# Performance work log

Measured on AMD Instinct MI355X. Metric: run time of the kernel, lower is better.

## Reference

```python
import jax, jax.numpy as jnp
import numpy as np

S, B, E, H, M = 1024, 4, 1024, 16, 128  # seq, batch, embed, heads, model_dims (key width)
V = E // H                              # value_dims = 64
_WSCALE = 1.0 / np.sqrt(E)              # keep softmax logits O(1)


def _cplx(re, im):
    return jax.lax.complex(re, im)


def setup_inputs() -> dict:
    key = jax.random.key(0)
    ks = jax.random.split(key, 10)
    n = lambda k, shp: jax.random.normal(k, shp, dtype=jnp.float32)
    w = lambda k, shp: n(k, shp) * np.float32(_WSCALE / np.sqrt(2.0))
    return {
        "logits_re": n(ks[0], (S, B, E)),
        "logits_im": n(ks[1], (S, B, E)),
        "wq_re": w(ks[2], (H, M, E)), "wq_im": w(ks[3], (H, M, E)),
        "wk_re": w(ks[4], (H, M, E)), "wk_im": w(ks[5], (H, M, E)),
        "wv_re": w(ks[6], (H, V, E)), "wv_im": w(ks[7], (H, V, E)),
        "wo_re": w(ks[8], (E, E)),    "wo_im": w(ks[9], (E, E)),
    }


def reference(logits_re, logits_im, wq_re, wq_im, wk_re, wk_im,
              wv_re, wv_im, wo_re, wo_im):
    x = _cplx(logits_re, logits_im)          # (s, b, e) complex64
    wq = _cplx(wq_re, wq_im)                 # (h, m, e)
    wk = _cplx(wk_re, wk_im)
    wv = _cplx(wv_re, wv_im)                 # (h, v, e)
    wo = _cplx(wo_re, wo_im)                 # (e, e)

    q = jnp.einsum('hme,sbe->bhsm', wq, x)   # (b, h, s, m)
    k = jnp.einsum('hme,sbe->bhsm', wk, x)
    v = jnp.einsum('hve,sbe->bhsv', wv, x)   # (b, h, s, v)

    scores = jnp.einsum('bhsm,bhtm->bhst', q, k)         # complex, no conjugation (matches torch matmul)
    amp = jnp.abs(scores)                                # -> float32
    causal = jnp.triu(jnp.ones((S, S), dtype=bool), 1)   # True above diagonal -> masked
    amp = jnp.where(causal, -jnp.inf, amp) / jnp.sqrt(jnp.float32(M))
    attn = jax.nn.softmax(amp, axis=-1).astype(scores.dtype)  # cast back to complex64

    upd = jnp.einsum('bhst,bhtv->bhsv', attn, v)         # (b, h, s, v)
    upd = upd.transpose(2, 0, 1, 3).reshape(S, B, E)     # 's2 b (h v)'
    out = jnp.einsum('sbe,ef->sbf', upd, wo) + x         # residual
    # complex output returned as stacked (real, imag) float32 for harness compatibility
    return jnp.stack([out.real, out.imag])
```

## Files before the change

kernel.cpp:

```cpp
#include <hip/hip_runtime.h>
#include <math.h>

#define S_DIM 1024
#define B_DIM 4
#define E_DIM 1024
#define H_DIM 16
#define M_DIM 128
#define V_DIM 64

typedef __attribute__((ext_vector_type(8))) short short8;
typedef __attribute__((ext_vector_type(4))) float f32x4;
typedef __attribute__((ext_vector_type(4))) int int4v;

__device__ __forceinline__ unsigned short f2bf(float f) {
    union { float f; unsigned u; } v; v.f = f;
    unsigned r = v.u + 0x7FFFu + ((v.u >> 16) & 1u);
    return (unsigned short)(r >> 16);
}

__device__ __forceinline__ void async16(const unsigned short* g, unsigned short* l) {
    __builtin_amdgcn_global_load_lds(
        (const __attribute__((address_space(1))) void*)g,
        (__attribute__((address_space(3))) void*)l,
        16, 0, 0);
}

__global__ __launch_bounds__(256) void convert_all(
    const float* __restrict__ xre,  const float* __restrict__ xim,
    const float* __restrict__ wqre, const float* __restrict__ wqim,
    const float* __restrict__ wkre, const float* __restrict__ wkim,
    const float* __restrict__ wvre, const float* __restrict__ wvim,
    unsigned short* __restrict__ xbre, unsigned short* __restrict__ xbim,
    unsigned short* __restrict__ wbre, unsigned short* __restrict__ wbim)
{
    const int i = blockIdx.x * 256 + threadIdx.x;
    const float *re, *im;
    unsigned short *dr, *di;
    int j;
    if (i < 1048576)      { re = xre;  im = xim;  dr = xbre;               di = xbim;               j = i; }
    else if (i < 1572864) { re = wqre; im = wqim; dr = wbre;               di = wbim;               j = i - 1048576; }
    else if (i < 2097152) { re = wkre; im = wkim; dr = wbre + 2048 * 1024; di = wbim + 2048 * 1024; j = i - 1572864; }
    else                  { re = wvre; im = wvim; dr = wbre + 4096 * 1024; di = wbim + 4096 * 1024; j = i - 2097152; }
    float4 r = ((const float4*)re)[j];
    float4 m = ((const float4*)im)[j];
    ushort4 ro, mo;
    ro.x = f2bf(r.x); ro.y = f2bf(r.y); ro.z = f2bf(r.z); ro.w = f2bf(r.w);
    mo.x = f2bf(m.x); mo.y = f2bf(m.y); mo.z = f2bf(m.z); mo.w = f2bf(m.w);
    ((ushort4*)dr)[j] = ro;
    ((ushort4*)di)[j] = mo;
}

__global__ __launch_bounds__(256) void transpose_wo(
    const float* __restrict__ wore, const float* __restrict__ woim,
    unsigned short* __restrict__ wtre, unsigned short* __restrict__ wtim)
{
    __shared__ float tr[32][33], ti[32][33];
    const int bx = blockIdx.x * 32;
    const int by = blockIdx.y * 32;
    const int tx = threadIdx.x & 31, ty = threadIdx.x >> 5;
    for (int i = ty; i < 32; i += 8) {
        tr[i][tx] = wore[(bx + i) * E_DIM + by + tx];
        ti[i][tx] = woim[(bx + i) * E_DIM + by + tx];
    }
    __syncthreads();
    for (int i = ty; i < 32; i += 8) {
        wtre[(by + i) * E_DIM + bx + tx] = f2bf(tr[tx][i]);
        wtim[(by + i) * E_DIM + bx + tx] = f2bf(ti[tx][i]);
    }
}

__global__ __launch_bounds__(256) void vtrans(
    const unsigned short* __restrict__ vrp, const unsigned short* __restrict__ vip,
    unsigned short* __restrict__ vrt, unsigned short* __restrict__ vit)
{
    __shared__ unsigned short tl[2][64][66];
    const int tid = threadIdx.x;
    const int t0 = blockIdx.x * 64;
    const int bh = blockIdx.y;
    #pragma unroll
    for (int pl = 0; pl < 2; ++pl) {
        const unsigned short* src = pl ? vip : vrp;
        #pragma unroll
        for (int p = 0; p < 2; ++p) {
            const int row = p * 32 + (tid >> 3);
            const int col = (tid & 7) * 8;
            short8 d = *(const short8*)&src[((size_t)bh * S_DIM + t0 + row) * V_DIM + col];
            #pragma unroll
            for (int j = 0; j < 8; ++j) tl[pl][row][col + j] = (unsigned short)d[j];
        }
    }
    __syncthreads();
    #pragma unroll
    for (int pl = 0; pl < 2; ++pl) {
        unsigned short* dst = pl ? vit : vrt;
        #pragma unroll
        for (int p = 0; p < 2; ++p) {
            const int v = p * 32 + (tid >> 3);
            const int tc = (tid & 7) * 8;
            short8 d;
            #pragma unroll
            for (int j = 0; j < 8; ++j) d[j] = (short)tl[pl][tc + j][v];
            *(short8*)&dst[((size_t)bh * V_DIM + v) * S_DIM + t0 + tc] = d;
        }
    }
}

template<int MODE>
__global__ __launch_bounds__(256, MODE ? 3 : 2) void cgemm(
    const unsigned short* __restrict__ Are, const unsigned short* __restrict__ Aim,
    const unsigned short* __restrict__ Bre, const unsigned short* __restrict__ Bim,
    unsigned short* __restrict__ qrp, unsigned short* __restrict__ qip,
    unsigned short* __restrict__ krp, unsigned short* __restrict__ kip,
    unsigned short* __restrict__ vrp, unsigned short* __restrict__ vip,
    const float* __restrict__ xre, const float* __restrict__ xim,
    float* __restrict__ out)
{
    constexpr int BM  = MODE ? 64 : 128;
    constexpr int IM  = MODE ? 2 : 4;
    constexpr int ASZ = BM * 32;
    constexpr int BUF = 2 * ASZ + 8192;
    __shared__ __align__(16) unsigned short lds[2 * BUF];
    const int tid  = threadIdx.x;
    const int wave = tid >> 6;
    const int lane = tid & 63;
    const int r0 = blockIdx.x * BM;
    const int j0 = blockIdx.y * 128;
    const int wm = (wave >> 1) * (MODE ? 32 : 64);
    const int wn = (wave & 1) * 64;

    f32x4 accre[IM][4], accim[IM][4];
    #pragma unroll
    for (int i = 0; i < IM; ++i)
        #pragma unroll
        for (int j = 0; j < 4; ++j) {
            accre[i][j] = (f32x4){0.f, 0.f, 0.f, 0.f};
            accim[i][j] = (f32x4){0.f, 0.f, 0.f, 0.f};
        }

    const int sr   = tid >> 2;
    const int sc   = (tid & 3) * 8;
    const int scol = ((tid & 3) ^ ((tid >> 3) & 3)) * 8;

    const int fr = lane & 15;
    const int xc = ((lane >> 4) ^ ((lane >> 1) & 3)) * 8;

    #define STAGE(sl, bb) { \
        const int kg = (sl) * 32; \
        unsigned short* b_ = &lds[(bb) * BUF]; \
        const size_t ga0 = (size_t)(r0 + sr) * E_DIM + kg + scol; \
        const size_t gb0 = (size_t)(j0 + sr) * E_DIM + kg + scol; \
        const size_t gb1 = (size_t)(j0 + 64 + sr) * E_DIM + kg + scol; \
        async16(Are + ga0, b_ + sr * 32 + sc); \
        async16(Aim + ga0, b_ + ASZ + sr * 32 + sc); \
        if (MODE == 0) { \
            const size_t ga1 = (size_t)(r0 + 64 + sr) * E_DIM + kg + scol; \
            async16(Are + ga1, b_ + (64 + sr) * 32 + sc); \
            async16(Aim + ga1, b_ + ASZ + (64 + sr) * 32 + sc); \
        } \
        async16(Bre + gb0, b_ + 2 * ASZ + sr * 32 + sc); \
        async16(Bre + gb1, b_ + 2 * ASZ + (64 + sr) * 32 + sc); \
        async16(Bim + gb0, b_ + 2 * ASZ + 4096 + sr * 32 + sc); \
        async16(Bim + gb1, b_ + 2 * ASZ + 4096 + (64 + sr) * 32 + sc); }

    STAGE(0, 0)
    asm volatile("s_waitcnt vmcnt(0)" ::: "memory");
    __builtin_amdgcn_s_barrier();

    #pragma unroll 1
    for (int s = 0; s < 32; ++s) {
        if (s < 31) STAGE(s + 1, (s + 1) & 1)

        const unsigned short* buf = &lds[(s & 1) * BUF];
        short8 ar[IM], ai[IM];
        #pragma unroll
        for (int im = 0; im < IM; ++im) {
            const int ro = (wm + im * 16 + fr) * 32 + xc;
            ar[im] = *(const short8*)&buf[ro];
            ai[im] = *(const short8*)&buf[ASZ + ro];
        }
        #pragma unroll
        for (int jn = 0; jn < 4; ++jn) {
            const int ro = (wn + jn * 16 + fr) * 32 + xc;
            const short8 br = *(const short8*)&buf[2 * ASZ + ro];
            const short8 bi = *(const short8*)&buf[2 * ASZ + 4096 + ro];
            int4v t = *(int4v*)&bi;
            t = t ^ (int)0x80008000;
            const short8 bin = *(short8*)&t;
            #pragma unroll
            for (int im = 0; im < IM; ++im) {
                accre[im][jn] = __builtin_amdgcn_mfma_f32_16x16x32_bf16(ar[im], br,  accre[im][jn], 0, 0, 0);
                accre[im][jn] = __builtin_amdgcn_mfma_f32_16x16x32_bf16(ai[im], bin, accre[im][jn], 0, 0, 0);
                accim[im][jn] = __builtin_amdgcn_mfma_f32_16x16x32_bf16(ar[im], bi,  accim[im][jn], 0, 0, 0);
                accim[im][jn] = __builtin_amdgcn_mfma_f32_16x16x32_bf16(ai[im], br,  accim[im][jn], 0, 0, 0);
            }
        }

        if (s < 31) {
            asm volatile("s_waitcnt vmcnt(0)" ::: "memory");
            __builtin_amdgcn_s_barrier();
        }
    }
    #undef STAGE

    const float qscale = 0.088388347648318447f;
    #pragma unroll
    for (int im = 0; im < IM; ++im) {
        #pragma unroll
        for (int reg = 0; reg < 4; ++reg) {
            const int r = r0 + wm + im * 16 + (lane >> 4) * 4 + reg;
            #pragma unroll
            for (int jn = 0; jn < 4; ++jn) {
                const int j = j0 + wn + jn * 16 + fr;
                const float vr = accre[im][jn][reg];
                const float vi = accim[im][jn][reg];
                if (MODE == 0) {
                    const int s = r >> 2, b = r & 3;
                    if (j < 2048) {
                        const int h = j >> 7, m = j & 127;
                        const size_t off = ((size_t)(b * H_DIM + h) * S_DIM + s) * M_DIM + m;
                        qrp[off] = f2bf(vr * qscale); qip[off] = f2bf(vi * qscale);
                    } else if (j < 4096) {
                        const int jl = j - 2048, h = jl >> 7, m = jl & 127;
                        const size_t off = ((size_t)(b * H_DIM + h) * S_DIM + s) * M_DIM + m;
                        krp[off] = f2bf(vr); kip[off] = f2bf(vi);
                    } else {
                        const int jl = j - 4096, h = jl >> 6, vv = jl & 63;
                        const size_t off = ((size_t)(b * H_DIM + h) * S_DIM + s) * V_DIM + vv;
                        vrp[off] = f2bf(vr); vip[off] = f2bf(vi);
                    }
                } else {
                    const int idx = r * E_DIM + j;
                    out[idx] = vr + xre[idx];
                    out[S_DIM * B_DIM * E_DIM + idx] = vi + xim[idx];
                }
            }
        }
    }
}

__global__ __launch_bounds__(512, 4) void attn_mfma(
    const unsigned short* __restrict__ qr, const unsigned short* __restrict__ qi,
    const unsigned short* __restrict__ kr, const unsigned short* __restrict__ ki,
    const unsigned short* __restrict__ vrt, const unsigned short* __restrict__ vit,
    unsigned short* __restrict__ updre, unsigned short* __restrict__ updim)
{
    __shared__ __align__(16) unsigned short Ks[2][64][136];
    __shared__ __align__(16) unsigned short Vs[2][64][72];
    __shared__ __align__(16) unsigned short Ps[8][16][88];

    const int tid  = threadIdx.x;
    const int wave = tid >> 6;
    const int lane = tid & 63;

    const int n  = blockIdx.x + 8 * blockIdx.y;
    const int bh = (n & 7) + 8 * (n >> 6);
    const int qt = 7 - ((n >> 3) & 7);

    const int q0 = qt * 128;
    const size_t base_qk = (size_t)bh * S_DIM * M_DIM;
    const size_t base_v  = (size_t)bh * V_DIM * S_DIM;

    const int fr = lane & 15;
    const int fg = lane >> 4;
    const int fk = fg * 8;

    const int krow = tid >> 4, kcol = (tid & 15) * 8;
    const int vrow = tid >> 3, vcol = (tid & 7) * 8;

    short8 Bqr[4], Bqi[4];
    {
        const size_t qo = base_qk + (size_t)(q0 + wave * 16 + fr) * M_DIM + fk;
        #pragma unroll
        for (int ks = 0; ks < 4; ++ks) {
            Bqr[ks] = *(const short8*)&qr[qo + ks * 32];
            Bqi[ks] = *(const short8*)&qi[qo + ks * 32];
        }
    }

    f32x4 Ore[4], Oim[4];
    #pragma unroll
    for (int vt = 0; vt < 4; ++vt) {
        Ore[vt] = (f32x4){0.f, 0.f, 0.f, 0.f};
        Oim[vt] = (f32x4){0.f, 0.f, 0.f, 0.f};
    }
    float mrun = -INFINITY, lrun = 0.f;
    const int qglob = q0 + wave * 16 + fr;
    const int qcap  = q0 + (wave >> 2) * 64;

    short8 pk[2][2], pv[2];
    #pragma unroll
    for (int pl = 0; pl < 2; ++pl) {
        const unsigned short* src = pl ? ki : kr;
        #pragma unroll
        for (int p = 0; p < 2; ++p)
            pk[pl][p] = *(const short8*)&src[base_qk + (size_t)(p * 32 + krow) * M_DIM + kcol];
    }
    #pragma unroll
    for (int pl = 0; pl < 2; ++pl) {
        const unsigned short* src = pl ? vit : vrt;
        pv[pl] = *(const short8*)&src[base_v + (size_t)vrow * S_DIM + vcol];
    }

    for (int t0 = 0; t0 <= q0 + 64; t0 += 64) {
        __syncthreads();
        #pragma unroll
        for (int pl = 0; pl < 2; ++pl) {
            #pragma unroll
            for (int p = 0; p < 2; ++p)
                *(short8*)&Ks[pl][p * 32 + krow][kcol] = pk[pl][p];
            *(short8*)&Vs[pl][vrow][vcol] = pv[pl];
        }
        __syncthreads();

        if (t0 <= q0) {
            const int tn = t0 + 64;
            #pragma unroll
            for (int pl = 0; pl < 2; ++pl) {
                const unsigned short* src = pl ? ki : kr;
                #pragma unroll
                for (int p = 0; p < 2; ++p)
                    pk[pl][p] = *(const short8*)&src[base_qk + (size_t)(tn + p * 32 + krow) * M_DIM + kcol];
            }
            #pragma unroll
            for (int pl = 0; pl < 2; ++pl) {
                const unsigned short* src = pl ? vit : vrt;
                pv[pl] = *(const short8*)&src[base_v + (size_t)vrow * S_DIM + tn + vcol];
            }
        }

        if (t0 > qcap) continue;

        f32x4 Sre[4], Sim[4];
        __builtin_amdgcn_s_setprio(1);
        #pragma unroll
        for (int tt = 0; tt < 4; ++tt) {
            Sre[tt] = (f32x4){0.f, 0.f, 0.f, 0.f};
            Sim[tt] = (f32x4){0.f, 0.f, 0.f, 0.f};
            const int trow = tt * 16 + fr;
            #pragma unroll
            for (int ks = 0; ks < 4; ++ks) {
                const short8 Akr = *(const short8*)&Ks[0][trow][ks * 32 + fk];
                const short8 Aki = *(const short8*)&Ks[1][trow][ks * 32 + fk];
                int4v t = *(int4v*)&Aki;
                t = t ^ (int)0x80008000;
                const short8 Akin = *(short8*)&t;
                Sre[tt] = __builtin_amdgcn_mfma_f32_16x16x32_bf16(Akr,  Bqr[ks], Sre[tt], 0, 0, 0);
                Sre[tt] = __builtin_amdgcn_mfma_f32_16x16x32_bf16(Akin, Bqi[ks], Sre[tt], 0, 0, 0);
                Sim[tt] = __builtin_amdgcn_mfma_f32_16x16x32_bf16(Akr,  Bqi[ks], Sim[tt], 0, 0, 0);
                Sim[tt] = __builtin_amdgcn_mfma_f32_16x16x32_bf16(Aki,  Bqr[ks], Sim[tt], 0, 0, 0);
            }
        }
        __builtin_amdgcn_s_setprio(0);

        float rowmax = -INFINITY;
        #pragma unroll
        for (int tt = 0; tt < 4; ++tt) {
            #pragma unroll
            for (int r = 0; r < 4; ++r) {
                const int tg = t0 + tt * 16 + fg * 4 + r;
                const float re = Sre[tt][r], im = Sim[tt][r];
                const float a = sqrtf(re * re + im * im);
                const float av = (tg > qglob) ? -INFINITY : a;
                Sre[tt][r] = av;
                rowmax = fmaxf(rowmax, av);
            }
        }
        rowmax = fmaxf(rowmax, __shfl_xor(rowmax, 16));
        rowmax = fmaxf(rowmax, __shfl_xor(rowmax, 32));

        if (!__all(rowmax - mrun <= 8.0f)) {
            const float nm = fmaxf(mrun, rowmax);
            const float alpha = __expf(mrun - nm);
            mrun = nm;
            lrun *= alpha;
            #pragma unroll
            for (int vt = 0; vt < 4; ++vt)
                #pragma unroll
                for (int r = 0; r < 4; ++r) { Ore[vt][r] *= alpha; Oim[vt][r] *= alpha; }
        }

        float psum = 0.f;
        #pragma unroll
        for (int tt = 0; tt < 4; ++tt) {
            const float p0 = __expf(Sre[tt][0] - mrun);
            const float p1 = __expf(Sre[tt][1] - mrun);
            const float p2 = __expf(Sre[tt][2] - mrun);
            const float p3 = __expf(Sre[tt][3] - mrun);
            psum += p0 + p1 + p2 + p3;
            ushort4 pw;
            pw.x = f2bf(p0); pw.y = f2bf(p1); pw.z = f2bf(p2); pw.w = f2bf(p3);
            *(ushort4*)&Ps[wave][fr][tt * 16 + fg * 4] = pw;
        }
        psum += __shfl_xor(psum, 16);
        psum += __shfl_xor(psum, 32);
        lrun += psum;

        const short8 Bp0 = *(const short8*)&Ps[wave][fr][fk];
        const short8 Bp1 = *(const short8*)&Ps[wave][fr][32 + fk];
        __builtin_amdgcn_s_setprio(1);
        #pragma unroll
        for (int vt = 0; vt < 4; ++vt) {
            const int vr2 = vt * 16 + fr;
            const short8 Ar0 = *(const short8*)&Vs[0][vr2][fk];
            const short8 Ar1 = *(const short8*)&Vs[0][vr2][32 + fk];
            const short8 Ai0 = *(const short8*)&Vs[1][vr2][fk];
            const short8 Ai1 = *(const short8*)&Vs[1][vr2][32 + fk];
            Ore[vt] = __builtin_amdgcn_mfma_f32_16x16x32_bf16(Ar0, Bp0, Ore[vt], 0, 0, 0);
            Ore[vt] = __builtin_amdgcn_mfma_f32_16x16x32_bf16(Ar1, Bp1, Ore[vt], 0, 0, 0);
            Oim[vt] = __builtin_amdgcn_mfma_f32_16x16x32_bf16(Ai0, Bp0, Oim[vt], 0, 0, 0);
            Oim[vt] = __builtin_amdgcn_mfma_f32_16x16x32_bf16(Ai1, Bp1, Oim[vt], 0, 0, 0);
        }
        __builtin_amdgcn_s_setprio(0);
    }

    const int b = bh >> 4, h = bh & 15;
    const float inv = 1.0f / lrun;
    const size_t base = ((size_t)(qglob * B_DIM + b)) * E_DIM + h * V_DIM;
    #pragma unroll
    for (int vt = 0; vt < 4; ++vt) {
        ushort4 pr, pi;
        pr.x = f2bf(Ore[vt][0] * inv); pr.y = f2bf(Ore[vt][1] * inv);
        pr.z = f2bf(Ore[vt][2] * inv); pr.w = f2bf(Ore[vt][3] * inv);
        pi.x = f2bf(Oim[vt][0] * inv); pi.y = f2bf(Oim[vt][1] * inv);
        pi.z = f2bf(Oim[vt][2] * inv); pi.w = f2bf(Oim[vt][3] * inv);
        *(ushort4*)&updre[base + vt * 16 + fg * 4] = pr;
        *(ushort4*)&updim[base + vt * 16 + fg * 4] = pi;
    }
}

extern "C" void kernel_launch(void* const* d_in, const int* in_sizes, int n_in,
                              void* d_out, int out_size, void* d_ws, size_t ws_size,
                              hipStream_t stream) {
    const float* xre  = (const float*)d_in[0];
    const float* xim  = (const float*)d_in[1];
    const float* wqre = (const float*)d_in[2];
    const float* wqim = (const float*)d_in[3];
    const float* wkre = (const float*)d_in[4];
    const float* wkim = (const float*)d_in[5];
    const float* wvre = (const float*)d_in[6];
    const float* wvim = (const float*)d_in[7];
    const float* wore = (const float*)d_in[8];
    const float* woim = (const float*)d_in[9];
    float* out = (float*)d_out;

    char* p = (char*)d_ws;
    const size_t QK = (size_t)B_DIM * H_DIM * S_DIM * M_DIM;
    const size_t VS = (size_t)B_DIM * H_DIM * S_DIM * V_DIM;
    const size_t SBE = (size_t)S_DIM * B_DIM * E_DIM;
    unsigned short* qrw = (unsigned short*)p;  p += QK * 2;
    unsigned short* qiw = (unsigned short*)p;  p += QK * 2;
    unsigned short* krw = (unsigned short*)p;  p += QK * 2;
    unsigned short* kiw = (unsigned short*)p;  p += QK * 2;
    unsigned short* vrw = (unsigned short*)p;  p += VS * 2;
    unsigned short* viw = (unsigned short*)p;  p += VS * 2;
    unsigned short* vrt = (unsigned short*)p;  p += VS * 2;
    unsigned short* vit = (unsigned short*)p;  p += VS * 2;
    unsigned short* updre = (unsigned short*)p; p += SBE * 2;
    unsigned short* updim = (unsigned short*)p; p += SBE * 2;
    unsigned short* xbre  = (unsigned short*)p; p += SBE * 2;
    unsigned short* xbim  = (unsigned short*)p; p += SBE * 2;
    unsigned short* wbre  = (unsigned short*)p; p += (size_t)5120 * E_DIM * 2;
    unsigned short* wbim  = (unsigned short*)p; p += (size_t)5120 * E_DIM * 2;
    unsigned short* wtre  = (unsigned short*)p; p += (size_t)E_DIM * E_DIM * 2;
    unsigned short* wtim  = (unsigned short*)p; p += (size_t)E_DIM * E_DIM * 2;

    convert_all<<<9216, 256, 0, stream>>>(xre, xim, wqre, wqim, wkre, wkim, wvre, wvim,
                                          xbre, xbim, wbre, wbim);
    transpose_wo<<<dim3(32, 32), 256, 0, stream>>>(wore, woim, wtre, wtim);

    cgemm<0><<<dim3(32, 40), 256, 0, stream>>>(xbre, xbim, wbre, wbim,
                                               qrw, qiw, krw, kiw, vrw, viw,
                                               nullptr, nullptr, nullptr);
    vtrans<<<dim3(16, 64), 256, 0, stream>>>(vrw, viw, vrt, vit);
    attn_mfma<<<dim3(8, 64), 512, 0, stream>>>(qrw, qiw, krw, kiw, vrt, vit, updre, updim);
    cgemm<1><<<dim3(64, 8), 256, 0, stream>>>(updre, updim, wtre, wtim,
                                              nullptr, nullptr, nullptr, nullptr, nullptr, nullptr,
                                              xre, xim, out);
}
```

Baseline: 484.7 us.

## Retile causal attention to 64-query blocks with double-buffered swizzled LDS

Shrinks the attention block from 128 queries and 8 waves to 64 queries and 4 waves, and steps keys 32 at a time instead of 64. This doubles the grid and gives finer causal skipping per wave. K and V tiles move to double-buffered LDS with an XOR swizzle instead of padding, which cuts the loop to one barrier per iteration and aims to avoid bank conflicts. The smaller tiles mean more iterations and less K/V reuse per block, and launch bounds change to 256 threads with 3 blocks.

After: 428.3 us (median of 2 runs). -11.6%, faster.

```diff
diff --git a/kernel.cpp b/kernel.cpp
--- a/kernel.cpp
+++ b/kernel.cpp
@@ -238,25 +238,26 @@
     }
 }
 
-__global__ __launch_bounds__(512, 4) void attn_mfma(
+__global__ __launch_bounds__(256, 3) void attn_mfma(
     const unsigned short* __restrict__ qr, const unsigned short* __restrict__ qi,
     const unsigned short* __restrict__ kr, const unsigned short* __restrict__ ki,
     const unsigned short* __restrict__ vrt, const unsigned short* __restrict__ vit,
     unsigned short* __restrict__ updre, unsigned short* __restrict__ updim)
 {
-    __shared__ __align__(16) unsigned short Ks[2][64][136];
-    __shared__ __align__(16) unsigned short Vs[2][64][72];
-    __shared__ __align__(16) unsigned short Ps[8][16][88];
+    __shared__ __align__(16) unsigned short Ks[2][2][32][128];
+    __shared__ __align__(16) unsigned short Vs[2][2][64][32];
+    __shared__ __align__(16) unsigned short Ps[4][16][32];
 
     const int tid  = threadIdx.x;
     const int wave = tid >> 6;
     const int lane = tid & 63;
 
-    const int n  = blockIdx.x + 8 * blockIdx.y;
-    const int bh = (n & 7) + 8 * (n >> 6);
-    const int qt = 7 - ((n >> 3) & 7);
-
-    const int q0 = qt * 128;
+    const int n  = blockIdx.x + 16 * blockIdx.y;
+    const int m_ = n >> 3;
+    const int bh = (n & 7) + 8 * (m_ >> 4);
+    const int qt = 15 - (m_ & 15);
+
+    const int q0 = qt * 64;
     const size_t base_qk = (size_t)bh * S_DIM * M_DIM;
     const size_t base_v  = (size_t)bh * V_DIM * S_DIM;
 
@@ -264,8 +265,10 @@
     const int fg = lane >> 4;
     const int fk = fg * 8;
 
-    const int krow = tid >> 4, kcol = (tid & 15) * 8;
-    const int vrow = tid >> 3, vcol = (tid & 7) * 8;
+    const int krow = tid >> 4;
+    const int kch  = tid & 15;
+    const int vrow = tid >> 2;
+    const int vch  = tid & 3;
 
     short8 Bqr[4], Bqi[4];
     {
@@ -285,7 +288,7 @@
     }
     float mrun = -INFINITY, lrun = 0.f;
     const int qglob = q0 + wave * 16 + fr;
-    const int qcap  = q0 + (wave >> 2) * 64;
+    const int qcap  = q0 + wave * 16 + 15;
 
     short8 pk[2][2], pv[2];
     #pragma unroll
@@ -293,54 +296,52 @@
         const unsigned short* src = pl ? ki : kr;
         #pragma unroll
         for (int p = 0; p < 2; ++p)
-            pk[pl][p] = *(const short8*)&src[base_qk + (size_t)(p * 32 + krow) * M_DIM + kcol];
-    }
-    #pragma unroll
-    for (int pl = 0; pl < 2; ++pl) {
-        const unsigned short* src = pl ? vit : vrt;
-        pv[pl] = *(const short8*)&src[base_v + (size_t)vrow * S_DIM + vcol];
-    }
-
-    for (int t0 = 0; t0 <= q0 + 64; t0 += 64) {
-        __syncthreads();
+            pk[pl][p] = *(const short8*)&src[base_qk + (size_t)(p * 16 + krow) * M_DIM + kch * 8];
+        const unsigned short* vsrc = pl ? vit : vrt;
+        pv[pl] = *(const short8*)&vsrc[base_v + (size_t)vrow * S_DIM + vch * 8];
+    }
+
+    const int tmax = q0 + 32;
+    for (int t0 = 0; t0 <= tmax; t0 += 32) {
+        const int bf = (t0 >> 5) & 1;
         #pragma unroll
         for (int pl = 0; pl < 2; ++pl) {
             #pragma unroll
-            for (int p = 0; p < 2; ++p)
-                *(short8*)&Ks[pl][p * 32 + krow][kcol] = pk[pl][p];
-            *(short8*)&Vs[pl][vrow][vcol] = pv[pl];
-        }
-        __syncthreads();
-
-        if (t0 <= q0) {
-            const int tn = t0 + 64;
+            for (int p = 0; p < 2; ++p) {
+                const int row = p * 16 + krow;
+                *(short8*)&Ks[bf][pl][row][(kch ^ (row & 7)) << 3] = pk[pl][p];
+            }
+            *(short8*)&Vs[bf][pl][vrow][(vch ^ ((vrow >> 1) & 3)) << 3] = pv[pl];
+        }
+        if (t0 < tmax) {
+            const int tn = t0 + 32;
             #pragma unroll
             for (int pl = 0; pl < 2; ++pl) {
                 const unsigned short* src = pl ? ki : kr;
                 #pragma unroll
                 for (int p = 0; p < 2; ++p)
-                    pk[pl][p] = *(const short8*)&src[base_qk + (size_t)(tn + p * 32 + krow) * M_DIM + kcol];
-            }
-            #pragma unroll
-            for (int pl = 0; pl < 2; ++pl) {
-                const unsigned short* src = pl ? vit : vrt;
-                pv[pl] = *(const short8*)&src[base_v + (size_t)vrow * S_DIM + tn + vcol];
-            }
-        }
+                    pk[pl][p] = *(const short8*)&src[base_qk + (size_t)(tn + p * 16 + krow) * M_DIM + kch * 8];
+                const unsigned short* vsrc = pl ? vit : vrt;
+                pv[pl] = *(const short8*)&vsrc[base_v + (size_t)vrow * S_DIM + tn + vch * 8];
+            }
+        }
+        __syncthreads();
 
         if (t0 > qcap) continue;
 
-        f32x4 Sre[4], Sim[4];
+        f32x4 Sre[2], Sim[2];
         __builtin_amdgcn_s_setprio(1);
         #pragma unroll
-        for (int tt = 0; tt < 4; ++tt) {
+        for (int tt = 0; tt < 2; ++tt) {
             Sre[tt] = (f32x4){0.f, 0.f, 0.f, 0.f};
             Sim[tt] = (f32x4){0.f, 0.f, 0.f, 0.f};
             const int trow = tt * 16 + fr;
+            const int sw = trow & 7;
             #pragma unroll
             for (int ks = 0; ks < 4; ++ks) {
-                const short8 Akr = *(const short8*)&Ks[0][trow][ks * 32 + fk];
-                const short8 Aki = *(const short8*)&Ks[1][trow][ks * 32 + fk];
+                const int off = ((ks * 4 + fg) ^ sw) << 3;
+                const short8 Akr = *(const short8*)&Ks[bf][0][trow][off];
+                const short8 Aki = *(const short8*)&Ks[bf][1][trow][off];
                 int4v t = *(int4v*)&Aki;
                 t = t ^ (int)0x80008000;
                 const short8 Akin = *(short8*)&t;
@@ -354,7 +355,7 @@
 
         float rowmax = -INFINITY;
         #pragma unroll
-        for (int tt = 0; tt < 4; ++tt) {
+        for (int tt = 0; tt < 2; ++tt) {
             #pragma unroll
             for (int r = 0; r < 4; ++r) {
                 const int tg = t0 + tt * 16 + fg * 4 + r;
@@ -380,8 +381,9 @@
         }
 
         float psum = 0.f;
-        #pragma unroll
-        for (int tt = 0; tt < 4; ++tt) {
+        const int psw = (fr >> 1) & 3;
+        #pragma unroll
+        for (int tt = 0; tt < 2; ++tt) {
             const float p0 = __expf(Sre[tt][0] - mrun);
             const float p1 = __expf(Sre[tt][1] - mrun);
             const float p2 = __expf(Sre[tt][2] - mrun);
@@ -389,26 +391,23 @@
             psum += p0 + p1 + p2 + p3;
             ushort4 pw;
             pw.x = f2bf(p0); pw.y = f2bf(p1); pw.z = f2bf(p2); pw.w = f2bf(p3);
-            *(ushort4*)&Ps[wave][fr][tt * 16 + fg * 4] = pw;
+            const int poff = (((tt * 2 + (fg >> 1)) ^ psw) << 3) + (fg & 1) * 4;
+            *(ushort4*)&Ps[wave][fr][poff] = pw;
         }
         psum += __shfl_xor(psum, 16);
         psum += __shfl_xor(psum, 32);
         lrun += psum;
 
-        const short8 Bp0 = *(const short8*)&Ps[wave][fr][fk];
-        const short8 Bp1 = *(const short8*)&Ps[wave][fr][32 + fk];
+        const short8 Bp = *(const short8*)&Ps[wave][fr][(fg ^ psw) << 3];
         __builtin_amdgcn_s_setprio(1);
         #pragma unroll
         for (int vt = 0; vt < 4; ++vt) {
             const int vr2 = vt * 16 + fr;
-            const short8 Ar0 = *(const short8*)&Vs[0][vr2][fk];
-            const short8 Ar1 = *(const short8*)&Vs[0][vr2][32 + fk];
-            const short8 Ai0 = *(const short8*)&Vs[1][vr2][fk];
-            const short8 Ai1 = *(const short8*)&Vs[1][vr2][32 + fk];
-            Ore[vt] = __builtin_amdgcn_mfma_f32_16x16x32_bf16(Ar0, Bp0, Ore[vt], 0, 0, 0);
-            Ore[vt] = __builtin_amdgcn_mfma_f32_16x16x32_bf16(Ar1, Bp1, Ore[vt], 0, 0, 0);
-            Oim[vt] = __builtin_amdgcn_mfma_f32_16x16x32_bf16(Ai0, Bp0, Oim[vt], 0, 0, 0);
-            Oim[vt] = __builtin_amdgcn_mfma_f32_16x16x32_bf16(Ai1, Bp1, Oim[vt], 0, 0, 0);
+            const int voff = (fg ^ ((vr2 >> 1) & 3)) << 3;
+            const short8 Ar = *(const short8*)&Vs[bf][0][vr2][voff];
+            const short8 Ai = *(const short8*)&Vs[bf][1][vr2][voff];
+            Ore[vt] = __builtin_amdgcn_mfma_f32_16x16x32_bf16(Ar, Bp, Ore[vt], 0, 0, 0);
+            Oim[vt] = __builtin_amdgcn_mfma_f32_16x16x32_bf16(Ai, Bp, Oim[vt], 0, 0, 0);
         }
         __builtin_amdgcn_s_setprio(0);
     }
@@ -472,7 +471,7 @@
                                                qrw, qiw, krw, kiw, vrw, viw,
                                                nullptr, nullptr, nullptr);
     vtrans<<<dim3(16, 64), 256, 0, stream>>>(vrw, viw, vrt, vit);
-    attn_mfma<<<dim3(8, 64), 512, 0, stream>>>(qrw, qiw, krw, kiw, vrt, vit, updre, updim);
+    attn_mfma<<<dim3(16, 64), 256, 0, stream>>>(qrw, qiw, krw, kiw, vrt, vit, updre, updim);
     cgemm<1><<<dim3(64, 8), 256, 0, stream>>>(updre, updim, wtre, wtim,
                                               nullptr, nullptr, nullptr, nullptr, nullptr, nullptr,
                                               xre, xim, out);
```
